# Optimization experiments

Hardware: AMD Instinct MI355X
Metric: run time of the kernel (lower is better)

## Reference

```python
import jax, jax.numpy as jnp
import numpy as np

B, N, C, H = 16, 1024, 768, 12
HD = C // H               # head_dim = 64
SCALE = HD ** -0.5
EPS = 1e-5


def ter_quant(w):
    """BitNet-b1.58 ternary weight quantization with straight-through estimator.
    Per-tensor scale = mean(|W|); weights rounded to {-1,0,1}*scale."""
    s = jnp.mean(jnp.abs(w))
    wq = jnp.round(jnp.clip(w / (s + EPS), -1.0, 1.0)) * s
    return w + jax.lax.stop_gradient(wq - w)


def setup_inputs() -> dict:
    key = jax.random.key(0)
    k1, k2, k3 = jax.random.split(key, 3)
    return {
        "x": jax.random.normal(k1, (B, N, C), dtype=jnp.float32),
        "w_qkv": jax.random.normal(k2, (3 * C, C), dtype=jnp.float32) * 0.02,
        "w_proj": jax.random.normal(k3, (C, C), dtype=jnp.float32) * 0.02,
        "b_proj": jnp.zeros((C,), dtype=jnp.float32),
    }


def reference(x, w_qkv, w_proj, b_proj):
    # ternary-quantized QKV projection: [B,N,C] @ [C,3C] -> [B,N,3C]
    qkv = jnp.einsum('bnc,dc->bnd', x, ter_quant(w_qkv))
    qkv = qkv.reshape(B, N, 3, H, HD).transpose(2, 0, 3, 1, 4)  # [3,B,H,N,HD]
    q, k, v = qkv[0], qkv[1], qkv[2]
    # manual softmax attention (dropout p=0 -> identity)
    attn = jax.nn.softmax(jnp.einsum('bhqd,bhkd->bhqk', q, k) * SCALE, axis=-1)
    out = jnp.einsum('bhqk,bhkd->bhqd', attn, v)          # [B,H,N,HD]
    out = out.transpose(0, 2, 1, 3).reshape(B, N, C)      # [B,N,C]
    # ternary-quantized output projection
    return jnp.einsum('bnc,dc->bnd', out, ter_quant(w_proj)) + b_proj
```

## Files before the change

### kernel.cpp

```cpp
#include <hip/hip_runtime.h>
#include <hip/hip_bf16.h>

#define DEVI __device__ __forceinline__

typedef __bf16 bf16_t;
typedef __bf16 bf16x8 __attribute__((ext_vector_type(8)));
typedef float  f32x4  __attribute__((ext_vector_type(4)));
typedef float  f32x16 __attribute__((ext_vector_type(16)));
typedef unsigned short u16x4 __attribute__((ext_vector_type(4)));
typedef unsigned int   u32x4 __attribute__((ext_vector_type(4)));

typedef __attribute__((address_space(1))) unsigned int gas_u32;
typedef __attribute__((address_space(3))) unsigned int las_u32;

#define LOG2E 1.4426950408889634f

DEVI void gload16(const void* g, void* l) {
  __builtin_amdgcn_global_load_lds((gas_u32*)g, (las_u32*)l, 16, 0, 0);
}

DEVI unsigned short bf16bits(float f) {
  bf16_t b = (bf16_t)f;
  return __builtin_bit_cast(unsigned short, b);
}

DEVI unsigned pk2(float a, float b) {
  return ((unsigned)bf16bits(b) << 16) | (unsigned)bf16bits(a);
}

__global__ __launch_bounds__(256) void k_abssum(const float* __restrict__ w, int n,
                                                double* __restrict__ partials) {
  __shared__ double sm[256];
  const int t = threadIdx.x;
  double acc = 0.0;
  for (int i = blockIdx.x * 256 + t; i < n; i += 256 * 256)
    acc += (double)fabsf(w[i]);
  sm[t] = acc;
  __syncthreads();
  #pragma unroll
  for (int s = 128; s > 0; s >>= 1) {
    if (t < s) sm[t] += sm[t + s];
    __syncthreads();
  }
  if (t == 0) partials[blockIdx.x] = sm[0];
}

__global__ __launch_bounds__(256) void k_reduce2(const double* __restrict__ partials,
                                                 double* __restrict__ outs) {
  __shared__ double sm[256];
  const int t = threadIdx.x;
  sm[t] = partials[blockIdx.x * 256 + t];
  __syncthreads();
  #pragma unroll
  for (int s = 128; s > 0; s >>= 1) {
    if (t < s) sm[t] += sm[t + s];
    __syncthreads();
  }
  if (t == 0) outs[blockIdx.x] = sm[0];
}

__global__ __launch_bounds__(256) void k_quant(const float* __restrict__ w,
                                               const double* __restrict__ sum, double invn,
                                               bf16_t* __restrict__ out) {
  const double s = (*sum) * invn + 1e-5;
  const int i = blockIdx.x * 256 + threadIdx.x;
  double tq = (double)w[i] / s;
  tq = fmin(fmax(tq, -1.0), 1.0);
  out[i] = (bf16_t)(float)rint(tq);
}

__global__ __launch_bounds__(256) void k_tobf16(const float* __restrict__ x,
                                                bf16_t* __restrict__ y) {
  const int i = blockIdx.x * 256 + threadIdx.x;
  const float4 v = ((const float4*)x)[i];
  u16x4 pk = { bf16bits(v.x), bf16bits(v.y), bf16bits(v.z), bf16bits(v.w) };
  ((u16x4*)y)[i] = pk;
}

template<int MODE>
__global__ __launch_bounds__(512, 2) void k_gemm(
    const bf16_t* __restrict__ A, const bf16_t* __restrict__ Bw,
    const double* __restrict__ sumptr, double invn,
    bf16_t* __restrict__ Qb, bf16_t* __restrict__ Kb, bf16_t* __restrict__ VTb,
    const float* __restrict__ bias, float* __restrict__ Out,
    int nxblk)
{
  __shared__ __align__(16) char lds[147456];
  const int t = threadIdx.x, l = t & 63, w = t >> 6;

  const int nblk = nxblk * 64;
  const int flat = blockIdx.y * nxblk + blockIdx.x;
  const int per = nblk >> 3;
  const int swz = (flat & 7) * per + (flat >> 3);
  const int m0 = (swz / nxblk) * 256, n0 = (swz % nxblk) * 128;

  const int wm = w >> 1, wn = w & 1;
  const int srow = l >> 3, scol = (l & 7) * 8;
  const int lq = l & 15, lh = l >> 4;
  const int gcol = scol ^ (srow * 8);

  auto sA = [&](int slot, int kts, int ha, int c) {
    const int row = ha * 128 + (c * 8 + w) * 8 + srow;
    gload16(A + (size_t)(m0 + row) * 768 + kts * 64 + gcol,
            lds + slot * 49152 + ha * 16384 + (c * 8 + w) * 1024);
  };
  auto sB = [&](int slot, int kts, int c) {
    const int row = (c * 8 + w) * 8 + srow;
    gload16(Bw + (size_t)(n0 + row) * 768 + kts * 64 + gcol,
            lds + slot * 49152 + 32768 + (c * 8 + w) * 1024);
  };

  f32x4 acc[4][4] = {};

  sA(0, 0, 0, 0); sA(0, 0, 0, 1); sA(0, 0, 1, 0); sA(0, 0, 1, 1);
  sB(0, 0, 0);    sB(0, 0, 1);
  sA(1, 1, 0, 0); sA(1, 1, 0, 1); sA(1, 1, 1, 0); sA(1, 1, 1, 1);
  sB(1, 1, 0);    sB(1, 1, 1);
  asm volatile("s_waitcnt vmcnt(6)" ::: "memory");
  asm volatile("s_barrier" ::: "memory");

  #pragma unroll
  for (int kt = 0; kt < 12; ++kt) {
    const char* cA = lds + (kt % 3) * 49152;
    const char* cB = cA + 32768;
    const int st3 = (kt + 2) % 3;
    const bool stg = (kt < 10);

    {
      bf16x8 af[4], bf[4];
      #pragma unroll
      for (int i = 0; i < 4; ++i) {
        const int row = wm * 64 + i * 16 + lq;
        af[i] = *(const bf16x8*)(cA + row * 128 + ((lh * 16) ^ ((row & 7) << 4)));
      }
      #pragma unroll
      for (int j = 0; j < 4; ++j) {
        const int row = wn * 64 + j * 16 + lq;
        bf[j] = *(const bf16x8*)(cB + row * 128 + ((lh * 16) ^ ((row & 7) << 4)));
      }
      if (stg) { sA(st3, kt + 2, 0, 0); sA(st3, kt + 2, 0, 1); sB(st3, kt + 2, 0); }
      asm volatile("s_barrier" ::: "memory");
      __builtin_amdgcn_s_setprio(1);
      #pragma unroll
      for (int i = 0; i < 4; ++i)
        #pragma unroll
        for (int j = 0; j < 4; ++j)
          acc[i][j] = __builtin_amdgcn_mfma_f32_16x16x32_bf16(af[i], bf[j], acc[i][j], 0, 0, 0);
      __builtin_amdgcn_s_setprio(0);
      asm volatile("s_barrier" ::: "memory");
    }
    {
      bf16x8 af[4], bf[4];
      #pragma unroll
      for (int i = 0; i < 4; ++i) {
        const int row = wm * 64 + i * 16 + lq;
        af[i] = *(const bf16x8*)(cA + row * 128 + ((64 + lh * 16) ^ ((row & 7) << 4)));
      }
      #pragma unroll
      for (int j = 0; j < 4; ++j) {
        const int row = wn * 64 + j * 16 + lq;
        bf[j] = *(const bf16x8*)(cB + row * 128 + ((64 + lh * 16) ^ ((row & 7) << 4)));
      }
      if (stg) { sA(st3, kt + 2, 1, 0); sA(st3, kt + 2, 1, 1); sB(st3, kt + 2, 1); }
      asm volatile("s_barrier" ::: "memory");
      __builtin_amdgcn_s_setprio(1);
      #pragma unroll
      for (int i = 0; i < 4; ++i)
        #pragma unroll
        for (int j = 0; j < 4; ++j)
          acc[i][j] = __builtin_amdgcn_mfma_f32_16x16x32_bf16(af[i], bf[j], acc[i][j], 0, 0, 0);
      __builtin_amdgcn_s_setprio(0);
      if (stg) asm volatile("s_waitcnt vmcnt(6)" ::: "memory");
      else     asm volatile("s_waitcnt vmcnt(0)" ::: "memory");
      asm volatile("s_barrier" ::: "memory");
    }
  }

  const float s = (float)((*sumptr) * invn);
  char* st = lds + w * 8192;

  const int mrow0 = m0 + wm * 64;
  const int b = mrow0 >> 10, nbase = mrow0 & 1023;

  if (MODE == 0) {
    const int d0 = n0 + wn * 64;
    const int which = d0 / 768;
    const int hh = (d0 >> 6) % 12;
    if (which == 2) {
      #pragma unroll
      for (int j = 0; j < 4; ++j)
        #pragma unroll
        for (int i = 0; i < 4; ++i)
          #pragma unroll
          for (int r = 0; r < 4; ++r) {
            const int rowd = j * 16 + lq;
            const int coln = (i * 16 + lh * 4 + r) * 2;
            *(bf16_t*)(st + rowd * 128 + (coln ^ ((rowd & 7) << 4))) =
                (bf16_t)(acc[i][j][r] * s);
          }
    } else {
      const float sc = (which == 0) ? s * 0.125f * LOG2E : s;
      #pragma unroll
      for (int i = 0; i < 4; ++i)
        #pragma unroll
        for (int j = 0; j < 4; ++j)
          #pragma unroll
          for (int r = 0; r < 4; ++r) {
            const int row = i * 16 + lh * 4 + r;
            const int colb = (j * 16 + lq) * 2;
            *(bf16_t*)(st + row * 128 + (colb ^ ((row & 7) << 4))) =
                (bf16_t)(acc[i][j][r] * sc);
          }
    }
    __syncthreads();
    if (which == 2) {
      char* dstp = (char*)(VTb + ((size_t)(b * 12 + hh) * 64) * 1024 + nbase);
      #pragma unroll
      for (int it = 0; it < 8; ++it) {
        const int rowd = it * 8 + (l >> 3);
        const int coln = (l & 7) * 16;
        const u32x4 v = *(const u32x4*)(st + rowd * 128 + (coln ^ ((rowd & 7) << 4)));
        *(u32x4*)(dstp + rowd * 2048 + coln) = v;
      }
    } else {
      bf16_t* __restrict__ dst = (which == 0) ? Qb : Kb;
      char* dstp = (char*)(dst + ((size_t)(b * 12 + hh) * 1024 + nbase) * 64);
      #pragma unroll
      for (int it = 0; it < 8; ++it) {
        const int row = it * 8 + (l >> 3);
        const int colb = (l & 7) * 16;
        const u32x4 v = *(const u32x4*)(st + row * 128 + (colb ^ ((row & 7) << 4)));
        *(u32x4*)(dstp + row * 128 + colb) = v;
      }
    }
  } else {
    const int d0 = n0 + wn * 64;
    const float4 bv = *(const float4*)(bias + d0 + (l & 15) * 4);
    #pragma unroll
    for (int c = 0; c < 2; ++c) {
      #pragma unroll
      for (int i2 = 0; i2 < 2; ++i2) {
        const int i = c * 2 + i2;
        #pragma unroll
        for (int j = 0; j < 4; ++j)
          #pragma unroll
          for (int r = 0; r < 4; ++r) {
            const int row = i2 * 16 + lh * 4 + r;
            const int colb = (j * 16 + lq) * 4;
            *(float*)(st + row * 256 + (colb ^ ((row & 7) << 4))) = acc[i][j][r] * s;
          }
      }
      __syncthreads();
      #pragma unroll
      for (int it = 0; it < 8; ++it) {
        const int row = it * 4 + (l >> 4);
        const int colb = (l & 15) * 16;
        float4 v = *(const float4*)(st + row * 256 + (colb ^ ((row & 7) << 4)));
        v.x += bv.x; v.y += bv.y; v.z += bv.z; v.w += bv.w;
        *(float4*)((char*)(Out + (size_t)(mrow0 + c * 32 + row) * 768 + d0) + colb) = v;
      }
      __syncthreads();
    }
  }
}

__global__ __launch_bounds__(256, 3) void k_attn(
    const bf16_t* __restrict__ Qb, const bf16_t* __restrict__ Kb,
    const bf16_t* __restrict__ VTb, bf16_t* __restrict__ Ob)
{
  __shared__ bf16_t smem[2][2][4096];
  const int t = threadIdx.x, l = t & 63, w = t >> 6;
  const int bh = blockIdx.x, qb = blockIdx.y;
  const int lq = l & 31, hi = l >> 5;
  const int srow = l >> 3, scol = (l & 7) * 8;
  const int q0 = qb * 128 + w * 32;

  bf16x8 qf[4];
  #pragma unroll
  for (int ks = 0; ks < 4; ++ks)
    qf[ks] = *(const bf16x8*)(Qb + ((size_t)bh * 1024 + q0 + lq) * 64 + ks * 16 + hi * 8);

  f32x16 ot[2] = {};
  float mrun = -1e30f, lrun = 0.0f;

  auto stage = [&](int buf, int kt) {
    const int nn0 = kt * 64;
    #pragma unroll
    for (int i = 0; i < 2; ++i) {
      const int c = i * 4 + w;
      const int row = c * 8 + srow;
      const int gcol = scol ^ ((row & 7) * 8);
      gload16(Kb + ((size_t)bh * 1024 + nn0 + row) * 64 + gcol, &smem[buf][0][c * 512]);
      gload16(VTb + ((size_t)bh * 64 + row) * 1024 + nn0 + gcol, &smem[buf][1][c * 512]);
    }
  };

  stage(0, 0);
  __syncthreads();

  for (int kt = 0; kt < 16; ++kt) {
    const int cur = kt & 1;
    if (kt < 15) stage(cur ^ 1, kt + 1);
    const char* lK = (const char*)smem[cur][0];
    const char* lV = (const char*)smem[cur][1];

    f32x16 st[2] = {};
    __builtin_amdgcn_s_setprio(1);
    #pragma unroll
    for (int kt2 = 0; kt2 < 2; ++kt2) {
      #pragma unroll
      for (int ks = 0; ks < 4; ++ks) {
        const int row = kt2 * 32 + lq;
        const bf16x8 kf =
            *(const bf16x8*)(lK + row * 128 + ((ks * 32 + hi * 16) ^ ((row & 7) << 4)));
        st[kt2] = __builtin_amdgcn_mfma_f32_32x32x16_bf16(kf, qf[ks], st[kt2], 0, 0, 0);
      }
    }
    __builtin_amdgcn_s_setprio(0);

    float pmax = st[0][0];
    #pragma unroll
    for (int r = 1; r < 16; ++r) pmax = fmaxf(pmax, st[0][r]);
    #pragma unroll
    for (int r = 0; r < 16; ++r) pmax = fmaxf(pmax, st[1][r]);
    pmax = fmaxf(pmax, __shfl_xor(pmax, 32));

    if (__any(pmax > mrun + 8.0f)) {
      const float mn = fmaxf(mrun, pmax);
      const float corr = __builtin_amdgcn_exp2f(mrun - mn);
      lrun *= corr;
      #pragma unroll
      for (int dt = 0; dt < 2; ++dt)
        #pragma unroll
        for (int r = 0; r < 16; ++r) ot[dt][r] *= corr;
      mrun = mn;
    }

    float psum = 0.0f;
    __builtin_amdgcn_s_setprio(1);
    #pragma unroll
    for (int g = 0; g < 4; ++g) {
      const int tile = g >> 1, r0 = (g & 1) * 8;
      float p[8];
      #pragma unroll
      for (int e = 0; e < 8; ++e) {
        p[e] = __builtin_amdgcn_exp2f(st[tile][r0 + e] - mrun);
        psum += p[e];
      }
      const unsigned w0 = pk2(p[0], p[1]), w1 = pk2(p[2], p[3]);
      const unsigned w2 = pk2(p[4], p[5]), w3 = pk2(p[6], p[7]);
      const unsigned x0 = __shfl_xor(w0, 32), x1 = __shfl_xor(w1, 32);
      const unsigned x2 = __shfl_xor(w2, 32), x3 = __shfl_xor(w3, 32);
      const u32x4 fw = hi ? u32x4{x2, x3, w2, w3} : u32x4{w0, w1, x0, x1};
      const bf16x8 pf = __builtin_bit_cast(bf16x8, fw);
      #pragma unroll
      for (int dt = 0; dt < 2; ++dt) {
        const int row = dt * 32 + lq;
        const bf16x8 vf =
            *(const bf16x8*)(lV + row * 128 + ((g * 32 + hi * 16) ^ ((row & 7) << 4)));
        ot[dt] = __builtin_amdgcn_mfma_f32_32x32x16_bf16(vf, pf, ot[dt], 0, 0, 0);
      }
    }
    __builtin_amdgcn_s_setprio(0);
    psum += __shfl_xor(psum, 32);
    lrun += psum;

    __syncthreads();
  }

  __syncthreads();
  bf16_t* olds = (bf16_t*)smem + w * 2048;
  const float inv = 1.0f / lrun;
  #pragma unroll
  for (int dt = 0; dt < 2; ++dt)
    #pragma unroll
    for (int rg = 0; rg < 4; ++rg) {
      u16x4 pk;
      #pragma unroll
      for (int e = 0; e < 4; ++e) pk[e] = bf16bits(ot[dt][rg * 4 + e] * inv);
      const int d = rg * 8 + hi * 4 + dt * 32;
      *(u16x4*)((char*)olds + ((lq * 128 + d * 2) ^ ((lq & 7) << 4))) = pk;
    }
  __syncthreads();
  const int b = bh / 12, h = bh % 12;
  #pragma unroll
  for (int i = 0; i < 8; ++i) {
    const int q = i * 4 + (l >> 4);
    const u16x4 v =
        *(const u16x4*)((const char*)olds + ((q * 128 + (l & 15) * 8) ^ ((q & 7) << 4)));
    *(u16x4*)(Ob + ((size_t)(b * 1024 + q0 + q)) * 768 + h * 64 + (l & 15) * 4) = v;
  }
}

extern "C" void kernel_launch(void* const* d_in, const int* in_sizes, int n_in,
                              void* d_out, int out_size, void* d_ws, size_t ws_size,
                              hipStream_t stream) {
  const float* x      = (const float*)d_in[0];
  const float* w_qkv  = (const float*)d_in[1];
  const float* w_proj = (const float*)d_in[2];
  const float* b_proj = (const float*)d_in[3];
  float* out = (float*)d_out;

  char* ws = (char*)d_ws;
  double* part  = (double*)ws;
  double* scl   = (double*)(ws + 4096);
  bf16_t* xbf   = (bf16_t*)(ws + 4608);
  bf16_t* wqs   = (bf16_t*)(ws + 4608 + 25165824);
  bf16_t* wps   = (bf16_t*)(ws + 4608 + 25165824 + 3538944);
  bf16_t* qbuf  = (bf16_t*)(ws + 4608 + 25165824 + 3538944 + 1179648);
  bf16_t* kbuf  = qbuf + 12582912;
  bf16_t* vtbuf = kbuf + 12582912;
  bf16_t* aout  = xbf;

  k_abssum<<<256, 256, 0, stream>>>(w_qkv, 2304 * 768, part);
  k_abssum<<<256, 256, 0, stream>>>(w_proj, 768 * 768, part + 256);
  k_reduce2<<<2, 256, 0, stream>>>(part, scl);
  k_quant<<<6912, 256, 0, stream>>>(w_qkv, scl, 1.0 / 1769472.0, wqs);
  k_quant<<<2304, 256, 0, stream>>>(w_proj, scl + 1, 1.0 / 589824.0, wps);
  k_tobf16<<<12288, 256, 0, stream>>>(x, xbf);
  k_gemm<0><<<dim3(18, 64), 512, 0, stream>>>(xbf, wqs, scl, 1.0 / 1769472.0,
                                              qbuf, kbuf, vtbuf, nullptr, nullptr, 18);
  k_attn<<<dim3(192, 8), 256, 0, stream>>>(qbuf, kbuf, vtbuf, aout);
  k_gemm<1><<<dim3(6, 64), 512, 0, stream>>>(aout, wps, scl + 1, 1.0 / 589824.0,
                                             nullptr, nullptr, nullptr, b_proj, out, 6);
}
```

Baseline: 212.6 us.

## Load attention K/V fragments directly from global memory and fuse prep kernels

The attention kernel no longer stages K and V^T tiles into double-buffered LDS with barriers. Each wave now loads its MFMA fragments straight from global memory into registers, relying on L2/L1 to serve the data the four waves share. Separately, the two abs-sum kernels are merged into one launch, and the quantize and bf16 conversion kernels are fused into a single vectorized prep kernel. This trades LDS reuse and async prefetch for fewer barriers and launches, at the risk of exposed global-load latency and more cache traffic in the attention loop.

```diff
diff --git a/kernel.cpp b/kernel.cpp
--- a/kernel.cpp
+++ b/kernel.cpp
@@ -28,12 +28,22 @@
   return ((unsigned)bf16bits(b) << 16) | (unsigned)bf16bits(a);
 }
 
-__global__ __launch_bounds__(256) void k_abssum(const float* __restrict__ w, int n,
-                                                double* __restrict__ partials) {
+DEVI unsigned short quant1(float wv, double s) {
+  double tq = (double)wv / s;
+  tq = fmin(fmax(tq, -1.0), 1.0);
+  return __builtin_bit_cast(unsigned short, (bf16_t)(float)rint(tq));
+}
+
+__global__ __launch_bounds__(256) void k_abssum2(const float* __restrict__ wq,
+                                                 const float* __restrict__ wp,
+                                                 double* __restrict__ partials) {
   __shared__ double sm[256];
-  const int t = threadIdx.x;
+  const int t = threadIdx.x, bid = blockIdx.x;
+  const float* __restrict__ w = (bid < 256) ? wq : wp;
+  const int n = (bid < 256) ? 1769472 : 589824;
+  const int b0 = bid & 255;
   double acc = 0.0;
-  for (int i = blockIdx.x * 256 + t; i < n; i += 256 * 256)
+  for (int i = b0 * 256 + t; i < n; i += 65536)
     acc += (double)fabsf(w[i]);
   sm[t] = acc;
   __syncthreads();
@@ -42,7 +52,7 @@
     if (t < s) sm[t] += sm[t + s];
     __syncthreads();
   }
-  if (t == 0) partials[blockIdx.x] = sm[0];
+  if (t == 0) partials[bid] = sm[0];
 }
 
 __global__ __launch_bounds__(256) void k_reduce2(const double* __restrict__ partials,
@@ -59,22 +69,29 @@
   if (t == 0) outs[blockIdx.x] = sm[0];
 }
 
-__global__ __launch_bounds__(256) void k_quant(const float* __restrict__ w,
-                                               const double* __restrict__ sum, double invn,
-                                               bf16_t* __restrict__ out) {
-  const double s = (*sum) * invn + 1e-5;
-  const int i = blockIdx.x * 256 + threadIdx.x;
-  double tq = (double)w[i] / s;
-  tq = fmin(fmax(tq, -1.0), 1.0);
-  out[i] = (bf16_t)(float)rint(tq);
-}
-
-__global__ __launch_bounds__(256) void k_tobf16(const float* __restrict__ x,
-                                                bf16_t* __restrict__ y) {
-  const int i = blockIdx.x * 256 + threadIdx.x;
-  const float4 v = ((const float4*)x)[i];
-  u16x4 pk = { bf16bits(v.x), bf16bits(v.y), bf16bits(v.z), bf16bits(v.w) };
-  ((u16x4*)y)[i] = pk;
+__global__ __launch_bounds__(256) void k_prep(
+    const float* __restrict__ wq, const float* __restrict__ wp,
+    const float* __restrict__ x, const double* __restrict__ scl,
+    bf16_t* __restrict__ wqs, bf16_t* __restrict__ wps, bf16_t* __restrict__ xbf) {
+  const int bid = blockIdx.x, t = threadIdx.x;
+  if (bid < 1728) {
+    const double s = scl[0] * (1.0 / 1769472.0) + 1e-5;
+    const int i = bid * 256 + t;
+    const float4 v = ((const float4*)wq)[i];
+    u16x4 o = { quant1(v.x, s), quant1(v.y, s), quant1(v.z, s), quant1(v.w, s) };
+    ((u16x4*)wqs)[i] = o;
+  } else if (bid < 2304) {
+    const double s = scl[1] * (1.0 / 589824.0) + 1e-5;
+    const int i = (bid - 1728) * 256 + t;
+    const float4 v = ((const float4*)wp)[i];
+    u16x4 o = { quant1(v.x, s), quant1(v.y, s), quant1(v.z, s), quant1(v.w, s) };
+    ((u16x4*)wps)[i] = o;
+  } else {
+    const int i = (bid - 2304) * 256 + t;
+    const float4 v = ((const float4*)x)[i];
+    u16x4 pk = { bf16bits(v.x), bf16bits(v.y), bf16bits(v.z), bf16bits(v.w) };
+    ((u16x4*)xbf)[i] = pk;
+  }
 }
 
 template<int MODE>
@@ -268,61 +285,56 @@
     const bf16_t* __restrict__ Qb, const bf16_t* __restrict__ Kb,
     const bf16_t* __restrict__ VTb, bf16_t* __restrict__ Ob)
 {
-  __shared__ bf16_t smem[2][2][4096];
+  __shared__ bf16_t eplds[4][2048];
   const int t = threadIdx.x, l = t & 63, w = t >> 6;
   const int bh = blockIdx.x, qb = blockIdx.y;
   const int lq = l & 31, hi = l >> 5;
-  const int srow = l >> 3, scol = (l & 7) * 8;
   const int q0 = qb * 128 + w * 32;
 
+  const bf16_t* __restrict__ Kg = Kb + (size_t)bh * 65536;
+  const bf16_t* __restrict__ Vg = VTb + (size_t)bh * 65536;
+
   bf16x8 qf[4];
   #pragma unroll
   for (int ks = 0; ks < 4; ++ks)
-    qf[ks] = *(const bf16x8*)(Qb + ((size_t)bh * 1024 + q0 + lq) * 64 + ks * 16 + hi * 8);
-
-  f32x16 ot[2] = {};
+    qf[ks] = *(const bf16x8*)(Qb + (size_t)bh * 65536 + (q0 + lq) * 64 + ks * 16 + hi * 8);
+
+  f32x16 ot0 = {}, ot1 = {};
   float mrun = -1e30f, lrun = 0.0f;
 
-  auto stage = [&](int buf, int kt) {
+  for (int kt = 0; kt < 16; ++kt) {
     const int nn0 = kt * 64;
-    #pragma unroll
-    for (int i = 0; i < 2; ++i) {
-      const int c = i * 4 + w;
-      const int row = c * 8 + srow;
-      const int gcol = scol ^ ((row & 7) * 8);
-      gload16(Kb + ((size_t)bh * 1024 + nn0 + row) * 64 + gcol, &smem[buf][0][c * 512]);
-      gload16(VTb + ((size_t)bh * 64 + row) * 1024 + nn0 + gcol, &smem[buf][1][c * 512]);
-    }
-  };
-
-  stage(0, 0);
-  __syncthreads();
-
-  for (int kt = 0; kt < 16; ++kt) {
-    const int cur = kt & 1;
-    if (kt < 15) stage(cur ^ 1, kt + 1);
-    const char* lK = (const char*)smem[cur][0];
-    const char* lV = (const char*)smem[cur][1];
-
-    f32x16 st[2] = {};
+
+    const bf16_t* kp = Kg + (size_t)(nn0 + lq) * 64 + hi * 8;
+    bf16x8 kf0[4], kf1[4];
+    #pragma unroll
+    for (int ks = 0; ks < 4; ++ks) kf0[ks] = *(const bf16x8*)(kp + ks * 16);
+    #pragma unroll
+    for (int ks = 0; ks < 4; ++ks) kf1[ks] = *(const bf16x8*)(kp + 2048 + ks * 16);
+
+    f32x16 st0 = {}, st1 = {};
     __builtin_amdgcn_s_setprio(1);
     #pragma unroll
-    for (int kt2 = 0; kt2 < 2; ++kt2) {
-      #pragma unroll
-      for (int ks = 0; ks < 4; ++ks) {
-        const int row = kt2 * 32 + lq;
-        const bf16x8 kf =
-            *(const bf16x8*)(lK + row * 128 + ((ks * 32 + hi * 16) ^ ((row & 7) << 4)));
-        st[kt2] = __builtin_amdgcn_mfma_f32_32x32x16_bf16(kf, qf[ks], st[kt2], 0, 0, 0);
-      }
+    for (int ks = 0; ks < 4; ++ks) {
+      st0 = __builtin_amdgcn_mfma_f32_32x32x16_bf16(kf0[ks], qf[ks], st0, 0, 0, 0);
+      st1 = __builtin_amdgcn_mfma_f32_32x32x16_bf16(kf1[ks], qf[ks], st1, 0, 0, 0);
     }
     __builtin_amdgcn_s_setprio(0);
 
-    float pmax = st[0][0];
-    #pragma unroll
-    for (int r = 1; r < 16; ++r) pmax = fmaxf(pmax, st[0][r]);
-    #pragma unroll
-    for (int r = 0; r < 16; ++r) pmax = fmaxf(pmax, st[1][r]);
+    const bf16_t* vp = Vg + (size_t)lq * 1024 + nn0 + hi * 8;
+    bf16x8 vf0[4], vf1[4];
+    #pragma unroll
+    for (int g = 0; g < 4; ++g) {
+      vf0[g] = *(const bf16x8*)(vp + g * 16);
+      vf1[g] = *(const bf16x8*)(vp + 32768 + g * 16);
+    }
+
+    float m8[8];
+    #pragma unroll
+    for (int r = 0; r < 8; ++r)
+      m8[r] = fmaxf(fmaxf(st0[r], st0[r + 8]), fmaxf(st1[r], st1[r + 8]));
+    float pmax = fmaxf(fmaxf(fmaxf(m8[0], m8[1]), fmaxf(m8[2], m8[3])),
+                       fmaxf(fmaxf(m8[4], m8[5]), fmaxf(m8[6], m8[7])));
     pmax = fmaxf(pmax, __shfl_xor(pmax, 32));
 
     if (__any(pmax > mrun + 8.0f)) {
@@ -330,46 +342,36 @@
       const float corr = __builtin_amdgcn_exp2f(mrun - mn);
       lrun *= corr;
       #pragma unroll
-      for (int dt = 0; dt < 2; ++dt)
-        #pragma unroll
-        for (int r = 0; r < 16; ++r) ot[dt][r] *= corr;
+      for (int r = 0; r < 16; ++r) { ot0[r] *= corr; ot1[r] *= corr; }
       mrun = mn;
     }
 
     float psum = 0.0f;
     __builtin_amdgcn_s_setprio(1);
-    #pragma unroll
-    for (int g = 0; g < 4; ++g) {
-      const int tile = g >> 1, r0 = (g & 1) * 8;
+    auto grp = [&](const f32x16& stv, int r0, const bf16x8& va, const bf16x8& vb) {
       float p[8];
       #pragma unroll
-      for (int e = 0; e < 8; ++e) {
-        p[e] = __builtin_amdgcn_exp2f(st[tile][r0 + e] - mrun);
-        psum += p[e];
-      }
+      for (int e = 0; e < 8; ++e) p[e] = __builtin_amdgcn_exp2f(stv[r0 + e] - mrun);
+      psum += ((p[0] + p[1]) + (p[2] + p[3])) + ((p[4] + p[5]) + (p[6] + p[7]));
       const unsigned w0 = pk2(p[0], p[1]), w1 = pk2(p[2], p[3]);
       const unsigned w2 = pk2(p[4], p[5]), w3 = pk2(p[6], p[7]);
       const unsigned x0 = __shfl_xor(w0, 32), x1 = __shfl_xor(w1, 32);
       const unsigned x2 = __shfl_xor(w2, 32), x3 = __shfl_xor(w3, 32);
       const u32x4 fw = hi ? u32x4{x2, x3, w2, w3} : u32x4{w0, w1, x0, x1};
       const bf16x8 pf = __builtin_bit_cast(bf16x8, fw);
-      #pragma unroll
-      for (int dt = 0; dt < 2; ++dt) {
-        const int row = dt * 32 + lq;
-        const bf16x8 vf =
-            *(const bf16x8*)(lV + row * 128 + ((g * 32 + hi * 16) ^ ((row & 7) << 4)));
-        ot[dt] = __builtin_amdgcn_mfma_f32_32x32x16_bf16(vf, pf, ot[dt], 0, 0, 0);
-      }
-    }
+      ot0 = __builtin_amdgcn_mfma_f32_32x32x16_bf16(va, pf, ot0, 0, 0, 0);
+      ot1 = __builtin_amdgcn_mfma_f32_32x32x16_bf16(vb, pf, ot1, 0, 0, 0);
+    };
+    grp(st0, 0, vf0[0], vf1[0]);
+    grp(st0, 8, vf0[1], vf1[1]);
+    grp(st1, 0, vf0[2], vf1[2]);
+    grp(st1, 8, vf0[3], vf1[3]);
     __builtin_amdgcn_s_setprio(0);
     psum += __shfl_xor(psum, 32);
     lrun += psum;
-
-    __syncthreads();
-  }
-
-  __syncthreads();
-  bf16_t* olds = (bf16_t*)smem + w * 2048;
+  }
+
+  bf16_t* olds = eplds[w];
   const float inv = 1.0f / lrun;
   #pragma unroll
   for (int dt = 0; dt < 2; ++dt)
@@ -377,7 +379,8 @@
     for (int rg = 0; rg < 4; ++rg) {
       u16x4 pk;
       #pragma unroll
-      for (int e = 0; e < 4; ++e) pk[e] = bf16bits(ot[dt][rg * 4 + e] * inv);
+      for (int e = 0; e < 4; ++e)
+        pk[e] = bf16bits((dt ? ot1[rg * 4 + e] : ot0[rg * 4 + e]) * inv);
       const int d = rg * 8 + hi * 4 + dt * 32;
       *(u16x4*)((char*)olds + ((lq * 128 + d * 2) ^ ((lq & 7) << 4))) = pk;
     }
@@ -412,12 +415,9 @@
   bf16_t* vtbuf = kbuf + 12582912;
   bf16_t* aout  = xbf;
 
-  k_abssum<<<256, 256, 0, stream>>>(w_qkv, 2304 * 768, part);
-  k_abssum<<<256, 256, 0, stream>>>(w_proj, 768 * 768, part + 256);
+  k_abssum2<<<512, 256, 0, stream>>>(w_qkv, w_proj, part);
   k_reduce2<<<2, 256, 0, stream>>>(part, scl);
-  k_quant<<<6912, 256, 0, stream>>>(w_qkv, scl, 1.0 / 1769472.0, wqs);
-  k_quant<<<2304, 256, 0, stream>>>(w_proj, scl + 1, 1.0 / 589824.0, wps);
-  k_tobf16<<<12288, 256, 0, stream>>>(x, xbf);
+  k_prep<<<14592, 256, 0, stream>>>(w_qkv, w_proj, x, scl, wqs, wps, xbf);
   k_gemm<0><<<dim3(18, 64), 512, 0, stream>>>(xbf, wqs, scl, 1.0 / 1769472.0,
                                               qbuf, kbuf, vtbuf, nullptr, nullptr, 18);
   k_attn<<<dim3(192, 8), 256, 0, stream>>>(qbuf, kbuf, vtbuf, aout);
```

New measurement: 299.5 us. +40.9%, slower.
